# Performance work log

Measured on AMD Instinct MI355X. Metric: run time of the kernel, lower is better.

Reference implementation:

```python
import jax, jax.numpy as jnp
import numpy as np


def setup_inputs() -> dict:
    key = jax.random.key(0)
    k1, k2 = jax.random.split(key)
    B, N, C = 32, 1024, 384
    x = jax.random.normal(k1, (B, N, C), dtype=jnp.float32)
    duration = jax.random.randint(k2, (B, N), 0, 8, dtype=jnp.int64)
    return {"x": x, "duration": duration, "max_length": 4096}


def reference(x, duration, max_length):
    # x: [B, N, C], duration: [B, N] int, max_length: python int
    B, N, C = x.shape
    dur = jnp.maximum(duration, 0)                       # duration.clip(min=0)
    cum = jnp.cumsum(dur, axis=1)                        # [B, N] exclusive-end offsets
    total = cum[:, -1]                                   # [B] expanded lengths
    t = jnp.arange(max_length)                           # [L]
    # Output frame t of row b copies token idx where cum[idx-1] <= t < cum[idx]:
    # idx = searchsorted(cum, t, side='right')  (vectorized repeat_interleave gather)
    idx = jax.vmap(lambda c: jnp.searchsorted(c, t, side="right"))(cum)  # [B, L]
    idx = jnp.minimum(idx, N - 1)                        # clamp padding region
    out = jnp.take_along_axis(x, idx[:, :, None], axis=1)  # [B, L, C]
    mel_mask = t[None, :] < total[:, None]               # [B, L] bool
    out = out * mel_mask[:, :, None].astype(x.dtype)     # zero-pad tail (fix_length)
    return out, mel_mask
```

## Files before the change

### kernel.cpp

```cpp
#include <hip/hip_runtime.h>

#define BB 32
#define NN 1024
#define TT 4096
#define CC 384
#define C4 (CC/4)
#define RPB 64
#define BPB (TT/RPB)
#define THR 256

typedef float f4v __attribute__((ext_vector_type(4)));

__global__ __launch_bounds__(THR) void lr_fused(const int* __restrict__ duration,
                                                const float4* __restrict__ x4,
                                                float4* __restrict__ out4,
                                                float* __restrict__ mask) {
    __shared__ int cum[NN];
    __shared__ int wtot[4];
    __shared__ int ridx[RPB];

    const int b    = blockIdx.x / BPB;
    const int rblk = blockIdx.x % BPB;
    const int tid  = threadIdx.x;
    const int lane = tid & 63;
    const int wid  = tid >> 6;

    const int4 dv = ((const int4*)(duration + b * NN))[tid];
    int d0 = max(dv.x, 0), d1 = max(dv.y, 0), d2 = max(dv.z, 0), d3 = max(dv.w, 0);
    int p0 = d0, p1 = p0 + d1, p2 = p1 + d2, p3 = p2 + d3;

    int v = p3;
    #pragma unroll
    for (int off = 1; off < 64; off <<= 1) {
        int t = __shfl_up(v, off, 64);
        if (lane >= off) v += t;
    }
    if (lane == 63) wtot[wid] = v;
    __syncthreads();
    int woff = 0;
    #pragma unroll
    for (int w = 0; w < 4; ++w)
        if (w < wid) woff += wtot[w];
    int excl = woff + (v - p3);
    int4 cv = make_int4(excl + p0, excl + p1, excl + p2, excl + p3);
    ((int4*)cum)[tid] = cv;
    __syncthreads();

    const int total = cum[NN - 1];

    if (tid < RPB) {
        int row = rblk * RPB + tid;
        int id = -1;
        if (row < total) {
            int lo = 0, hi = NN - 1;
            #pragma unroll
            for (int it = 0; it < 10; ++it) {
                int mid = (lo + hi) >> 1;
                if (cum[mid] > row) hi = mid; else lo = mid + 1;
            }
            id = hi;
        }
        ridx[tid] = id;
        mask[(size_t)b * TT + row] = (id >= 0) ? 1.0f : 0.0f;
    }
    __syncthreads();

    const float4* xb = x4 + (size_t)b * NN * C4;
    float4* ob = out4 + ((size_t)b * TT + (size_t)rblk * RPB) * C4;
    #pragma unroll
    for (int it = 0; it < RPB * C4 / THR; ++it) {
        int i = it * THR + tid;
        int r = i / C4;
        int lane2 = i - r * C4;
        int id = ridx[r];
        float4 vv = make_float4(0.f, 0.f, 0.f, 0.f);
        if (id >= 0) vv = xb[(size_t)id * C4 + lane2];
        __builtin_nontemporal_store(*(const f4v*)&vv, (f4v*)&ob[i]);
    }
}

extern "C" void kernel_launch(void* const* d_in, const int* in_sizes, int n_in,
                              void* d_out, int out_size, void* d_ws, size_t ws_size,
                              hipStream_t stream) {
    const float* x        = (const float*)d_in[0];
    const int*   duration = (const int*)d_in[1];

    float* out  = (float*)d_out;
    float* mask = out + (size_t)BB * TT * CC;

    lr_fused<<<BB * BPB, THR, 0, stream>>>(duration, (const float4*)x,
                                           (float4*)out, mask);
}
```

Before: 46.78 us.

## Replace binary search with scatter of token indices and double rows per block

Each thread now writes its own token index directly into the rows it covers, so the 10-step shared-memory binary search per row is gone. The total comes from the warp sums, which lets the mask write happen before the second barrier. Blocks grow to 512 threads and 128 rows each, which halves the number of blocks that each redo the duration prefix scan. The cost is fewer blocks (1024), a scatter loop whose length depends on duration, and a partial unroll of the copy loop.

```diff
diff --git a/kernel.cpp b/kernel.cpp
--- a/kernel.cpp
+++ b/kernel.cpp
@@ -5,9 +5,9 @@
 #define TT 4096
 #define CC 384
 #define C4 (CC/4)
-#define RPB 64
+#define RPB 128
 #define BPB (TT/RPB)
-#define THR 256
+#define THR 512
 
 typedef float f4v __attribute__((ext_vector_type(4)));
 
@@ -16,65 +16,65 @@
                                                 float4* __restrict__ out4,
                                                 float* __restrict__ mask) {
     __shared__ int cum[NN];
-    __shared__ int wtot[4];
+    __shared__ int wsum[8];
     __shared__ int ridx[RPB];
 
-    const int b    = blockIdx.x / BPB;
-    const int rblk = blockIdx.x % BPB;
+    const int b    = blockIdx.x >> 5;
+    const int rblk = blockIdx.x & (BPB - 1);
     const int tid  = threadIdx.x;
     const int lane = tid & 63;
     const int wid  = tid >> 6;
 
-    const int4 dv = ((const int4*)(duration + b * NN))[tid];
-    int d0 = max(dv.x, 0), d1 = max(dv.y, 0), d2 = max(dv.z, 0), d3 = max(dv.w, 0);
-    int p0 = d0, p1 = p0 + d1, p2 = p1 + d2, p3 = p2 + d3;
+    const int2 dv = ((const int2*)(duration + b * NN))[tid];
+    int d0 = max(dv.x, 0), d1 = max(dv.y, 0);
+    int ps = d0 + d1;
 
-    int v = p3;
+    int v = ps;
     #pragma unroll
     for (int off = 1; off < 64; off <<= 1) {
         int t = __shfl_up(v, off, 64);
         if (lane >= off) v += t;
     }
-    if (lane == 63) wtot[wid] = v;
+    if (lane == 63) wsum[wid] = v;
     __syncthreads();
-    int woff = 0;
+    int woff = 0, tot = 0;
     #pragma unroll
-    for (int w = 0; w < 4; ++w)
-        if (w < wid) woff += wtot[w];
-    int excl = woff + (v - p3);
-    int4 cv = make_int4(excl + p0, excl + p1, excl + p2, excl + p3);
-    ((int4*)cum)[tid] = cv;
+    for (int w = 0; w < 8; ++w) {
+        int s = wsum[w];
+        tot += s;
+        if (w < wid) woff += s;
+    }
+    const int excl = woff + (v - ps);
+    ((int2*)cum)[tid] = make_int2(excl + d0, excl + d0 + d1);
+
+    const int lo = rblk * RPB;
+    if (tid < RPB) {
+        ridx[tid] = -1;
+        mask[(size_t)b * TT + lo + tid] = (lo + tid < tot) ? 1.0f : 0.0f;
+    }
     __syncthreads();
 
-    const int total = cum[NN - 1];
-
-    if (tid < RPB) {
-        int row = rblk * RPB + tid;
-        int id = -1;
-        if (row < total) {
-            int lo = 0, hi = NN - 1;
-            #pragma unroll
-            for (int it = 0; it < 10; ++it) {
-                int mid = (lo + hi) >> 1;
-                if (cum[mid] > row) hi = mid; else lo = mid + 1;
-            }
-            id = hi;
-        }
-        ridx[tid] = id;
-        mask[(size_t)b * TT + row] = (id >= 0) ? 1.0f : 0.0f;
+    {
+        const int hi = lo + RPB;
+        int s0 = excl, e0 = excl + d0;
+        int a = max(s0, lo), e = min(e0, hi);
+        for (int t = a; t < e; ++t) ridx[t - lo] = 2 * tid;
+        int s1 = e0, e1 = e0 + d1;
+        a = max(s1, lo); e = min(e1, hi);
+        for (int t = a; t < e; ++t) ridx[t - lo] = 2 * tid + 1;
     }
     __syncthreads();
 
     const float4* xb = x4 + (size_t)b * NN * C4;
-    float4* ob = out4 + ((size_t)b * TT + (size_t)rblk * RPB) * C4;
-    #pragma unroll
+    float4* ob = out4 + ((size_t)b * TT + lo) * C4;
+    #pragma unroll 4
     for (int it = 0; it < RPB * C4 / THR; ++it) {
         int i = it * THR + tid;
         int r = i / C4;
-        int lane2 = i - r * C4;
+        int l2 = i - r * C4;
         int id = ridx[r];
         float4 vv = make_float4(0.f, 0.f, 0.f, 0.f);
-        if (id >= 0) vv = xb[(size_t)id * C4 + lane2];
+        if (id >= 0) vv = xb[(size_t)id * C4 + l2];
         __builtin_nontemporal_store(*(const f4v*)&vv, (f4v*)&ob[i]);
     }
 }
```

Result: slower. 47.74 us (+2.1%).
